# Optimization experiments

Hardware: AMD Instinct MI355X
Metric: run time of the kernel (lower is better)

Reference implementation:

```python
import jax, jax.numpy as jnp
import numpy as np

LN_EPS = 1e-5
NUM_HEADS = 16

def _layernorm(x, g, b):
    mu = jnp.mean(x, axis=-1, keepdims=True)
    var = jnp.mean(jnp.square(x - mu), axis=-1, keepdims=True)
    return (x - mu) * jax.lax.rsqrt(var + LN_EPS) * g + b

def setup_inputs() -> dict:
    key = jax.random.key(0)
    ks = jax.random.split(key, 8)
    B, N, C, Hf = 8, 4096, 1024, 2048
    s = 1.0 / np.sqrt(C)
    return {
        "x": jax.random.normal(ks[0], (B, N, C), jnp.float32),
        "ln1_g": jnp.ones((C,), jnp.float32),
        "ln1_b": jnp.zeros((C,), jnp.float32),
        "ln2_g": jnp.ones((C,), jnp.float32),
        "ln2_b": jnp.zeros((C,), jnp.float32),
        "wq": jax.random.normal(ks[1], (C, C), jnp.float32) * s,
        "wk": jax.random.normal(ks[2], (C, C), jnp.float32) * s,
        "wv": jax.random.normal(ks[3], (C, C), jnp.float32) * s,
        "proj_w": jax.random.normal(ks[4], (C, C), jnp.float32) * s,
        "proj_b": jnp.zeros((C,), jnp.float32),
        "fc1_w": jax.random.normal(ks[5], (C, Hf), jnp.float32) * s,
        "fc1_b": jnp.zeros((Hf,), jnp.float32),
        "fc2_w": jax.random.normal(ks[6], (Hf, C), jnp.float32) / np.sqrt(Hf),
        "fc2_b": jnp.zeros((C,), jnp.float32),
    }

def reference(x, ln1_g, ln1_b, ln2_g, ln2_b, wq, wk, wv, proj_w, proj_b,
              fc1_w, fc1_b, fc2_w, fc2_b):
    B, N, C = x.shape
    H = NUM_HEADS
    d = C // H
    scale = d ** -0.5

    # --- attention branch (note: attention over the head_dim axis, d x d scores) ---
    h = _layernorm(x, ln1_g, ln1_b)
    def split(t):  # (B,N,C) -> (B,H,d,N), matching permute(0,2,3,1)
        return jnp.transpose(t.reshape(B, N, H, d), (0, 2, 3, 1))
    q = split(h @ wq)
    k = split(h @ wk)
    v = split(h @ wv)
    attn = jax.nn.softmax(jnp.einsum("bhdn,bhen->bhde", q, k) * scale, axis=-1)  # (B,H,d,d)
    o = jnp.einsum("bhde,bhen->bhdn", attn, v)           # (B,H,d,N)
    o = jnp.transpose(o, (0, 2, 1, 3)).reshape(B, N, C)  # transpose(1,2).reshape
    x = x + (o @ proj_w + proj_b)

    # --- MLP branch ---
    h2 = _layernorm(x, ln2_g, ln2_b)
    h2 = jax.nn.gelu(h2 @ fc1_w + fc1_b, approximate=False)
    x = x + (h2 @ fc2_w + fc2_b)
    return x
```

## Files before the change

kernel.cpp:

```cpp
#include <hip/hip_runtime.h>
#include <cmath>

typedef __attribute__((ext_vector_type(8))) _Float16 f16x8;
typedef __attribute__((ext_vector_type(8))) unsigned short u16x8;
typedef __attribute__((ext_vector_type(4))) float f32x4;

__device__ __forceinline__ unsigned short f2h(float f) {
  return __builtin_bit_cast(unsigned short, (_Float16)f);
}
__device__ __forceinline__ float h2f(unsigned short u) {
  return (float)__builtin_bit_cast(_Float16, u);
}

__device__ __forceinline__ void async16(const void* gp, void* lp) {
  __builtin_amdgcn_global_load_lds(
      (const __attribute__((address_space(1))) void*)gp,
      (__attribute__((address_space(3))) void*)lp, 16, 0, 0);
}

__global__ __launch_bounds__(256) void transpose_cast(
    const float* __restrict__ W, unsigned short* __restrict__ WT, int K, int N) {
  __shared__ float tile[32][33];
  const int tx = threadIdx.x & 31, ty = threadIdx.x >> 5;
  const int n0 = blockIdx.x * 32, k0 = blockIdx.y * 32;
#pragma unroll
  for (int r = 0; r < 4; ++r)
    tile[ty + 8 * r][tx] = W[(size_t)(k0 + ty + 8 * r) * N + n0 + tx];
  __syncthreads();
#pragma unroll
  for (int r = 0; r < 4; ++r)
    WT[(size_t)(n0 + ty + 8 * r) * K + k0 + tx] = f2h(tile[tx][ty + 8 * r]);
}

__global__ __launch_bounds__(256) void layernorm_cast(
    const float* __restrict__ x, const float* __restrict__ g,
    const float* __restrict__ bt, unsigned short* __restrict__ out) {
  const int row = blockIdx.x, tid = threadIdx.x;
  const float4 v = ((const float4*)(x + (size_t)row * 1024))[tid];
  float s = v.x + v.y + v.z + v.w;
  float ss = v.x * v.x + v.y * v.y + v.z * v.z + v.w * v.w;
#pragma unroll
  for (int off = 32; off >= 1; off >>= 1) {
    s += __shfl_down(s, off);
    ss += __shfl_down(ss, off);
  }
  __shared__ float red[10];
  const int wave = tid >> 6, lane = tid & 63;
  if (lane == 0) { red[wave] = s; red[4 + wave] = ss; }
  __syncthreads();
  if (tid == 0) {
    float S = red[0] + red[1] + red[2] + red[3];
    float SS = red[4] + red[5] + red[6] + red[7];
    float mu = S * (1.f / 1024.f);
    float var = SS * (1.f / 1024.f) - mu * mu;
    red[8] = mu;
    red[9] = rsqrtf(var + 1e-5f);
  }
  __syncthreads();
  const float mu = red[8], rs = red[9];
  const float4 gv = ((const float4*)g)[tid];
  const float4 bv = ((const float4*)bt)[tid];
  ushort4 r;
  r.x = f2h((v.x - mu) * rs * gv.x + bv.x);
  r.y = f2h((v.y - mu) * rs * gv.y + bv.y);
  r.z = f2h((v.z - mu) * rs * gv.z + bv.z);
  r.w = f2h((v.w - mu) * rs * gv.w + bv.w);
  ((ushort4*)(out + (size_t)row * 1024))[tid] = r;
}

__global__ __launch_bounds__(256) void resid_ln(
    const float* __restrict__ x, const unsigned short* __restrict__ pr,
    const float* __restrict__ pb, const float* __restrict__ g,
    const float* __restrict__ bt, float* __restrict__ out,
    unsigned short* __restrict__ h2) {
  const int row = blockIdx.x, tid = threadIdx.x;
  const size_t off = (size_t)row * 1024;
  const float4 xv = ((const float4*)(x + off))[tid];
  const ushort4 pv = ((const ushort4*)(pr + off))[tid];
  const float4 bb = ((const float4*)pb)[tid];
  float4 v;
  v.x = xv.x + h2f(pv.x) + bb.x;
  v.y = xv.y + h2f(pv.y) + bb.y;
  v.z = xv.z + h2f(pv.z) + bb.z;
  v.w = xv.w + h2f(pv.w) + bb.w;
  ((float4*)(out + off))[tid] = v;
  float s = v.x + v.y + v.z + v.w;
  float ss = v.x * v.x + v.y * v.y + v.z * v.z + v.w * v.w;
#pragma unroll
  for (int o = 32; o >= 1; o >>= 1) {
    s += __shfl_down(s, o);
    ss += __shfl_down(ss, o);
  }
  __shared__ float red[10];
  const int wave = tid >> 6, lane = tid & 63;
  if (lane == 0) { red[wave] = s; red[4 + wave] = ss; }
  __syncthreads();
  if (tid == 0) {
    float S = red[0] + red[1] + red[2] + red[3];
    float SS = red[4] + red[5] + red[6] + red[7];
    float mu = S * (1.f / 1024.f);
    float var = SS * (1.f / 1024.f) - mu * mu;
    red[8] = mu;
    red[9] = rsqrtf(var + 1e-5f);
  }
  __syncthreads();
  const float mu = red[8], rs = red[9];
  const float4 gv = ((const float4*)g)[tid];
  const float4 bv = ((const float4*)bt)[tid];
  ushort4 r;
  r.x = f2h((v.x - mu) * rs * gv.x + bv.x);
  r.y = f2h((v.y - mu) * rs * gv.y + bv.y);
  r.z = f2h((v.z - mu) * rs * gv.z + bv.z);
  r.w = f2h((v.w - mu) * rs * gv.w + bv.w);
  ((ushort4*)(h2 + off))[tid] = r;
}

__global__ __launch_bounds__(256) void resid_add(
    float* __restrict__ out, const unsigned short* __restrict__ y,
    const float* __restrict__ b) {
  const int row = blockIdx.x, tid = threadIdx.x;
  const size_t off = (size_t)row * 1024;
  float4 o = ((const float4*)(out + off))[tid];
  const ushort4 yv = ((const ushort4*)(y + off))[tid];
  const float4 bv = ((const float4*)b)[tid];
  o.x += h2f(yv.x) + bv.x;
  o.y += h2f(yv.y) + bv.y;
  o.z += h2f(yv.z) + bv.z;
  o.w += h2f(yv.w) + bv.w;
  ((float4*)(out + off))[tid] = o;
}

__global__ __launch_bounds__(256) void gemm_bt(
    const unsigned short* __restrict__ A, const unsigned short* __restrict__ BT,
    int M, int N, int K,
    const float* __restrict__ bias, unsigned short* __restrict__ outB, int gelu) {
  __shared__ unsigned short smem[17408];
  unsigned short* sA = smem;
  unsigned short* sB = smem + 8192;
  const int tid = threadIdx.x, wave = tid >> 6, lane = tid & 63;
  const int l16 = lane & 15, g16 = lane >> 4;
  const int wm = wave & 1, wn = wave >> 1;

  const int lin = blockIdx.y * gridDim.x + blockIdx.x;
  const int t_ = lin >> 3;
  const int bx = t_ % gridDim.x;
  const int by = (lin & 7) + 8 * (t_ / gridDim.x);
  const int row0 = by * 128, col0 = bx * 128;

  const int r_ = tid >> 2;
  const int s_ = ((tid & 3) ^ ((tid >> 3) & 3)) * 8;
  const unsigned short* pA = A + (size_t)(row0 + r_) * K + s_;
  const unsigned short* pB = BT + (size_t)(col0 + r_) * K + s_;
  unsigned short* dA = sA + wave * 512;
  unsigned short* dB = sB + wave * 512;
  const size_t rstep = (size_t)64 * K;

  f32x4 acc[4][4] = {};

  for (int k0 = 0; k0 < K; k0 += 64) {
    __syncthreads();
    async16(pA, dA);
    async16(pA + rstep, dA + 2048);
    async16(pA + 32, dA + 4096);
    async16(pA + rstep + 32, dA + 6144);
    async16(pB, dB);
    async16(pB + rstep, dB + 2048);
    async16(pB + 32, dB + 4096);
    async16(pB + rstep + 32, dB + 6144);
    pA += 64;
    pB += 64;
    __syncthreads();
#pragma unroll
    for (int kk = 0; kk < 2; ++kk) {
      f16x8 af[4], bf[4];
#pragma unroll
      for (int i = 0; i < 4; ++i) {
        const int ra = wm * 64 + i * 16 + l16;
        af[i] = __builtin_bit_cast(f16x8,
            *(const u16x8*)&sA[kk * 4096 + ra * 32 + (g16 ^ ((ra >> 1) & 3)) * 8]);
      }
#pragma unroll
      for (int j = 0; j < 4; ++j) {
        const int rb = wn * 64 + j * 16 + l16;
        bf[j] = __builtin_bit_cast(f16x8,
            *(const u16x8*)&sB[kk * 4096 + rb * 32 + (g16 ^ ((rb >> 1) & 3)) * 8]);
      }
#pragma unroll
      for (int i = 0; i < 4; ++i)
#pragma unroll
        for (int j = 0; j < 4; ++j)
          acc[i][j] = __builtin_amdgcn_mfma_f32_16x16x32_f16(af[i], bf[j], acc[i][j], 0, 0, 0);
    }
  }

  __syncthreads();
  unsigned short* scr = smem + wave * 4352;
#pragma unroll
  for (int j = 0; j < 4; ++j) {
    const float bcol = gelu ? bias[col0 + wn * 64 + j * 16 + l16] : 0.f;
#pragma unroll
    for (int i = 0; i < 4; ++i)
#pragma unroll
      for (int r = 0; r < 4; ++r) {
        float val = acc[i][j][r] + bcol;
        if (gelu) val = 0.5f * val * (1.0f + erff(val * 0.70710678118f));
        scr[(i * 16 + g16 * 4 + r) * 68 + j * 16 + l16] = f2h(val);
      }
  }
#pragma unroll
  for (int rr = 0; rr < 8; ++rr) {
    const int lr = rr * 8 + (lane >> 3);
    const int lc = (lane & 7) * 8;
    const u16x8 val = *(const u16x8*)&scr[lr * 68 + lc];
    *(u16x8*)(outB + (size_t)(row0 + wm * 64 + lr) * N + col0 + wn * 64 + lc) = val;
  }
}

__global__ __launch_bounds__(256) void attn_qk_part(
    const unsigned short* __restrict__ qkv, float* __restrict__ sp) {
  constexpr int ST = 72;
  __shared__ unsigned short sQT[64 * ST];
  __shared__ unsigned short sKT[64 * ST];
  const int bx = blockIdx.x, bh = bx >> 2, chunk = bx & 3;
  const int b = bh >> 4, h = bh & 15;
  const size_t base = (size_t)b * 4096 * 3072 + (size_t)h * 64;
  const int tid = threadIdx.x, wave = tid >> 6, lane = tid & 63;
  const int l16 = lane & 15, g16 = lane >> 4;
  const int wm = wave & 1, wn = wave >> 1;
  const int srow = tid >> 2, sseg = tid & 3;

  f32x4 acc[2][2] = {};

  for (int ntl = 0; ntl < 16; ++ntl) {
    const int nt = chunk * 16 + ntl;
    __syncthreads();
    const size_t roff = base + (size_t)(nt * 64 + srow) * 3072 + sseg * 16;
    const u16x8 q0 = *(const u16x8*)(qkv + roff);
    const u16x8 q1 = *(const u16x8*)(qkv + roff + 8);
    const u16x8 k0 = *(const u16x8*)(qkv + roff + 1024);
    const u16x8 k1 = *(const u16x8*)(qkv + roff + 1032);
#pragma unroll
    for (int ii = 0; ii < 8; ++ii) {
      sQT[(sseg * 16 + ii) * ST + srow] = q0[ii];
      sQT[(sseg * 16 + 8 + ii) * ST + srow] = q1[ii];
      sKT[(sseg * 16 + ii) * ST + srow] = k0[ii];
      sKT[(sseg * 16 + 8 + ii) * ST + srow] = k1[ii];
    }
    __syncthreads();
#pragma unroll
    for (int kk = 0; kk < 2; ++kk) {
      f16x8 aq[2], bk[2];
#pragma unroll
      for (int i = 0; i < 2; ++i)
        aq[i] = __builtin_bit_cast(f16x8,
            *(const u16x8*)&sQT[(wm * 32 + i * 16 + l16) * ST + kk * 32 + g16 * 8]);
#pragma unroll
      for (int j = 0; j < 2; ++j)
        bk[j] = __builtin_bit_cast(f16x8,
            *(const u16x8*)&sKT[(wn * 32 + j * 16 + l16) * ST + kk * 32 + g16 * 8]);
#pragma unroll
      for (int i = 0; i < 2; ++i)
#pragma unroll
        for (int j = 0; j < 2; ++j)
          acc[i][j] = __builtin_amdgcn_mfma_f32_16x16x32_f16(aq[i], bk[j], acc[i][j], 0, 0, 0);
    }
  }

  float* o = sp + (size_t)bx * 4096;
#pragma unroll
  for (int i = 0; i < 2; ++i)
#pragma unroll
    for (int j = 0; j < 2; ++j)
#pragma unroll
      for (int r = 0; r < 4; ++r)
        o[(wm * 32 + i * 16 + g16 * 4 + r) * 64 + (wn * 32 + j * 16 + l16)] = acc[i][j][r];
}

__global__ __launch_bounds__(64) void attn_softmax(
    const float* __restrict__ sp, unsigned short* __restrict__ am) {
  const int bh = blockIdx.x, dd = threadIdx.x;
  const float* p = sp + (size_t)bh * 4 * 4096 + dd * 64;
  float row[64];
#pragma unroll
  for (int e4 = 0; e4 < 16; ++e4) {
    const float4 a = ((const float4*)p)[e4];
    const float4 b_ = ((const float4*)(p + 4096))[e4];
    const float4 c_ = ((const float4*)(p + 8192))[e4];
    const float4 d_ = ((const float4*)(p + 12288))[e4];
    row[4 * e4 + 0] = a.x + b_.x + c_.x + d_.x;
    row[4 * e4 + 1] = a.y + b_.y + c_.y + d_.y;
    row[4 * e4 + 2] = a.z + b_.z + c_.z + d_.z;
    row[4 * e4 + 3] = a.w + b_.w + c_.w + d_.w;
  }
  float mx = -1e30f;
#pragma unroll
  for (int e = 0; e < 64; ++e) mx = fmaxf(mx, row[e]);
  float sum = 0.f;
#pragma unroll
  for (int e = 0; e < 64; ++e) {
    row[e] = __expf(0.125f * (row[e] - mx));
    sum += row[e];
  }
  const float inv = 1.0f / sum;
  unsigned short* q = am + (size_t)bh * 4096 + dd * 64;
#pragma unroll
  for (int e = 0; e < 64; ++e) q[e] = f2h(row[e] * inv);
}

__global__ __launch_bounds__(256) void attn_pv(
    const unsigned short* __restrict__ qkv, const unsigned short* __restrict__ am,
    unsigned short* __restrict__ o) {
  const int bx = blockIdx.x, bh = bx >> 2, chunk = bx & 3;
  const int b = bh >> 4, h = bh & 15;
  const size_t base = (size_t)b * 4096 * 3072 + (size_t)h * 64;
  const int tid = threadIdx.x, wave = tid >> 6, lane = tid & 63;
  const int l16 = lane & 15, g16 = lane >> 4;
  const int wm = wave & 1, wn = wave >> 1;

  f16x8 amf[2][2];
#pragma unroll
  for (int i = 0; i < 2; ++i)
#pragma unroll
    for (int kk = 0; kk < 2; ++kk)
      amf[i][kk] = __builtin_bit_cast(f16x8,
          *(const u16x8*)(am + (size_t)bh * 4096 +
                          (wm * 32 + i * 16 + l16) * 64 + kk * 32 + g16 * 8));

  for (int ntl = 0; ntl < 16; ++ntl) {
    const int nt = chunk * 16 + ntl;
    f32x4 oc[2][2] = {};
#pragma unroll
    for (int kk = 0; kk < 2; ++kk) {
#pragma unroll
      for (int j = 0; j < 2; ++j) {
        const f16x8 vf = __builtin_bit_cast(f16x8,
            *(const u16x8*)(qkv + base + 2048 +
                            (size_t)(nt * 64 + wn * 32 + j * 16 + l16) * 3072 +
                            kk * 32 + g16 * 8));
#pragma unroll
        for (int i = 0; i < 2; ++i)
          oc[i][j] = __builtin_amdgcn_mfma_f32_16x16x32_f16(amf[i][kk], vf, oc[i][j], 0, 0, 0);
      }
    }
#pragma unroll
    for (int i = 0; i < 2; ++i)
#pragma unroll
      for (int j = 0; j < 2; ++j)
#pragma unroll
        for (int r = 0; r < 4; ++r) {
          const int dd = wm * 32 + i * 16 + g16 * 4 + r;
          const int nf = nt * 64 + wn * 32 + j * 16 + l16;
          const int row = b * 4096 + dd * 64 + h * 4 + (nf >> 10);
          o[(size_t)row * 1024 + (nf & 1023)] = f2h(oc[i][j][r]);
        }
  }
}

extern "C" void kernel_launch(void* const* d_in, const int* in_sizes, int n_in,
                              void* d_out, int out_size, void* d_ws, size_t ws_size,
                              hipStream_t stream) {
  (void)in_sizes; (void)n_in; (void)out_size; (void)ws_size;
  const float* x = (const float*)d_in[0];
  const float* ln1g = (const float*)d_in[1];
  const float* ln1b = (const float*)d_in[2];
  const float* ln2g = (const float*)d_in[3];
  const float* ln2b = (const float*)d_in[4];
  const float* wq = (const float*)d_in[5];
  const float* wk = (const float*)d_in[6];
  const float* wv = (const float*)d_in[7];
  const float* projw = (const float*)d_in[8];
  const float* projb = (const float*)d_in[9];
  const float* fc1w = (const float*)d_in[10];
  const float* fc1b = (const float*)d_in[11];
  const float* fc2w = (const float*)d_in[12];
  const float* fc2b = (const float*)d_in[13];
  float* out = (float*)d_out;

  const int M = 8 * 4096, C = 1024, HF = 2048;
  const size_t MC = (size_t)M * C;

  unsigned short* p = (unsigned short*)d_ws;
  unsigned short* wqkvT = p; p += (size_t)3 * C * C;
  unsigned short* prT = p; p += (size_t)C * C;
  unsigned short* f1T = p; p += (size_t)HF * C;
  unsigned short* f2T = p; p += (size_t)C * HF;
  unsigned short* hb = p;  p += MC;
  unsigned short* qkvb = p; p += 3 * MC;
  float* Spart = (float*)hb;
  unsigned short* Am = wqkvT;
  unsigned short* ob = hb;
  unsigned short* projout = qkvb;
  unsigned short* h2 = qkvb + 2 * MC;
  unsigned short* h3 = qkvb;
  unsigned short* yb = hb;

  transpose_cast<<<dim3(C / 32, C / 32), 256, 0, stream>>>(wq, wqkvT, C, C);
  transpose_cast<<<dim3(C / 32, C / 32), 256, 0, stream>>>(wk, wqkvT + (size_t)C * C, C, C);
  transpose_cast<<<dim3(C / 32, C / 32), 256, 0, stream>>>(wv, wqkvT + (size_t)2 * C * C, C, C);
  transpose_cast<<<dim3(C / 32, C / 32), 256, 0, stream>>>(projw, prT, C, C);
  transpose_cast<<<dim3(HF / 32, C / 32), 256, 0, stream>>>(fc1w, f1T, C, HF);
  transpose_cast<<<dim3(C / 32, HF / 32), 256, 0, stream>>>(fc2w, f2T, HF, C);

  layernorm_cast<<<M, 256, 0, stream>>>(x, ln1g, ln1b, hb);

  gemm_bt<<<dim3(3 * C / 128, M / 128), 256, 0, stream>>>(
      hb, wqkvT, M, 3 * C, C, nullptr, qkvb, 0);

  attn_qk_part<<<512, 256, 0, stream>>>(qkvb, Spart);
  attn_softmax<<<128, 64, 0, stream>>>(Spart, Am);
  attn_pv<<<512, 256, 0, stream>>>(qkvb, Am, ob);

  gemm_bt<<<dim3(C / 128, M / 128), 256, 0, stream>>>(
      ob, prT, M, C, C, nullptr, projout, 0);

  resid_ln<<<M, 256, 0, stream>>>(x, projout, projb, ln2g, ln2b, out, h2);

  gemm_bt<<<dim3(HF / 128, M / 128), 256, 0, stream>>>(
      h2, f1T, M, HF, C, fc1b, h3, 1);

  gemm_bt<<<dim3(C / 128, M / 128), 256, 0, stream>>>(
      h3, f2T, M, C, HF, nullptr, yb, 0);

  resid_add<<<M, 256, 0, stream>>>(out, yb, fc2b);
}
```

Baseline: 1.173 ms.

## Add 256x256-tile pipelined GEMM kernel for MLP fc1/fc2

Adds a new 512-thread GEMM kernel with 256x256 output tiles. It uses a double-buffered LDS pipeline fed by async global-to-LDS loads, swizzled LDS layout, block-index remapping for L2 locality, and setprio around the MFMA bursts. The two MLP GEMMs now launch this kernel instead of the 128x128 one, aiming for more data reuse per tile and better overlap of loads with compute. The larger tile uses 128KB of LDS and many accumulator registers, which limits occupancy, and it yields fewer blocks for the N=1024 fc2 GEMM.

```diff
diff --git a/kernel.cpp b/kernel.cpp
--- a/kernel.cpp
+++ b/kernel.cpp
@@ -213,6 +213,146 @@
     const int lc = (lane & 7) * 8;
     const u16x8 val = *(const u16x8*)&scr[lr * 68 + lc];
     *(u16x8*)(outB + (size_t)(row0 + wm * 64 + lr) * N + col0 + wn * 64 + lc) = val;
+  }
+}
+
+
+#define STAGE_A(TT, KKH)                                                       \
+  {                                                                            \
+    unsigned short* d = smem + ((TT) & 1) * 32768 + (KKH) * 8192 + wave * 512; \
+    const unsigned short* sp_ = pA + (size_t)(TT) * 64 + (KKH) * 32;           \
+    async16(sp_, d);                                                           \
+    async16(sp_ + rstep, d + 4096);                                            \
+  }
+
+#define STAGE_B(TT, KKH)                                                       \
+  {                                                                            \
+    unsigned short* d =                                                        \
+        smem + ((TT) & 1) * 32768 + 16384 + (KKH) * 8192 + wave * 512;         \
+    const unsigned short* sp_ = pB + (size_t)(TT) * 64 + (KKH) * 32;           \
+    async16(sp_, d);                                                           \
+    async16(sp_ + rstep, d + 4096);                                            \
+  }
+
+#define GPHASE(KK, MH, STAGE, TAILW)                                           \
+  {                                                                            \
+    f16x8 af[4];                                                               \
+    _Pragma("unroll") for (int i = 0; i < 4; ++i) {                            \
+      const int ra = wm * 128 + ((MH)*4 + i) * 16 + l16;                       \
+      af[i] = __builtin_bit_cast(                                              \
+          f16x8, *(const u16x8*)&bufA[(KK)*8192 + ra * 32 +                    \
+                                      ((g16 ^ ((ra >> 1) & 3)) * 8)]);         \
+    }                                                                          \
+    if ((MH) == 0) {                                                           \
+      _Pragma("unroll") for (int j = 0; j < 4; ++j) {                          \
+        const int rb = wn * 64 + j * 16 + l16;                                 \
+        bf[j] = __builtin_bit_cast(                                            \
+            f16x8, *(const u16x8*)&bufB[(KK)*8192 + rb * 32 +                  \
+                                        ((g16 ^ ((rb >> 1) & 3)) * 8)]);       \
+      }                                                                        \
+    }                                                                          \
+    STAGE;                                                                     \
+    __builtin_amdgcn_s_barrier();                                              \
+    asm volatile("s_waitcnt lgkmcnt(0)" ::: "memory");                         \
+    __builtin_amdgcn_s_setprio(1);                                             \
+    _Pragma("unroll") for (int i = 0; i < 4; ++i)                              \
+        _Pragma("unroll") for (int j = 0; j < 4; ++j) acc[(MH)*4 + i][j] =     \
+        __builtin_amdgcn_mfma_f32_16x16x32_f16(af[i], bf[j],                   \
+                                               acc[(MH)*4 + i][j], 0, 0, 0);   \
+    __builtin_amdgcn_s_setprio(0);                                             \
+    TAILW;                                                                     \
+    __builtin_amdgcn_s_barrier();                                              \
+  }
+
+__global__ __launch_bounds__(512) void gemm256(
+    const unsigned short* __restrict__ A, const unsigned short* __restrict__ BT,
+    int M, int N, int K,
+    const float* __restrict__ bias, unsigned short* __restrict__ outB, int gelu) {
+  __shared__ __align__(16) unsigned short smem[65536];
+  const int tid = threadIdx.x, wave = tid >> 6, lane = tid & 63;
+  const int l16 = lane & 15, g16 = lane >> 4;
+  const int wm = wave >> 2, wn = wave & 3;
+
+  const int lin = blockIdx.y * gridDim.x + blockIdx.x;
+  const int t_ = lin >> 3;
+  const int bx = t_ % gridDim.x;
+  const int by = (lin & 7) + 8 * (t_ / gridDim.x);
+  const int row0 = by * 256, col0 = bx * 256;
+
+  const int r_ = tid >> 2;
+  const int s_ = ((tid & 3) ^ ((tid >> 3) & 3)) * 8;
+  const unsigned short* pA = A + (size_t)(row0 + r_) * K + s_;
+  const unsigned short* pB = BT + (size_t)(col0 + r_) * K + s_;
+  const size_t rstep = (size_t)128 * K;
+  const int NT = K >> 6;
+
+  f32x4 acc[8][4] = {};
+
+  STAGE_B(0, 0);
+  STAGE_A(0, 0);
+  STAGE_B(0, 1);
+  STAGE_A(0, 1);
+  STAGE_B(1, 0);
+  STAGE_A(1, 0);
+  STAGE_B(1, 1);
+  asm volatile("s_waitcnt vmcnt(6)" ::: "memory");
+  __builtin_amdgcn_s_barrier();
+
+  for (int t = 0; t < NT - 2; ++t) {
+    const unsigned short* bufA = smem + (t & 1) * 32768;
+    const unsigned short* bufB = bufA + 16384;
+    f16x8 bf[4];
+    GPHASE(0, 0, STAGE_A(t + 1, 1), )
+    GPHASE(0, 1, STAGE_B(t + 2, 0), )
+    GPHASE(1, 0, STAGE_A(t + 2, 0), )
+    GPHASE(1, 1, STAGE_B(t + 2, 1),
+           asm volatile("s_waitcnt vmcnt(6)" ::: "memory"))
+  }
+
+  {
+    const int t = NT - 2;
+    const unsigned short* bufA = smem + (t & 1) * 32768;
+    const unsigned short* bufB = bufA + 16384;
+    f16x8 bf[4];
+    GPHASE(0, 0, STAGE_A(t + 1, 1), )
+    GPHASE(0, 1, , )
+    GPHASE(1, 0, , )
+    GPHASE(1, 1, , asm volatile("s_waitcnt vmcnt(0)" ::: "memory"))
+  }
+  {
+    const int t = NT - 1;
+    const unsigned short* bufA = smem + (t & 1) * 32768;
+    const unsigned short* bufB = bufA + 16384;
+    f16x8 bf[4];
+    GPHASE(0, 0, , )
+    GPHASE(0, 1, , )
+    GPHASE(1, 0, , )
+    GPHASE(1, 1, , )
+  }
+
+  unsigned short* scr = smem + wave * 4352;
+#pragma unroll
+  for (int mh = 0; mh < 2; ++mh) {
+#pragma unroll
+    for (int j = 0; j < 4; ++j) {
+      const float bcol = gelu ? bias[col0 + wn * 64 + j * 16 + l16] : 0.f;
+#pragma unroll
+      for (int i = 0; i < 4; ++i)
+#pragma unroll
+        for (int r = 0; r < 4; ++r) {
+          float val = acc[mh * 4 + i][j][r] + bcol;
+          if (gelu) val = 0.5f * val * (1.0f + erff(val * 0.70710678118f));
+          scr[(i * 16 + g16 * 4 + r) * 68 + j * 16 + l16] = f2h(val);
+        }
+    }
+#pragma unroll
+    for (int rr = 0; rr < 8; ++rr) {
+      const int lr = rr * 8 + (lane >> 3);
+      const int lc = (lane & 7) * 8;
+      const u16x8 val = *(const u16x8*)&scr[lr * 68 + lc];
+      *(u16x8*)(outB + (size_t)(row0 + wm * 128 + mh * 64 + lr) * N + col0 +
+                wn * 64 + lc) = val;
+    }
   }
 }
 
@@ -415,10 +555,10 @@
 
   resid_ln<<<M, 256, 0, stream>>>(x, projout, projb, ln2g, ln2b, out, h2);
 
-  gemm_bt<<<dim3(HF / 128, M / 128), 256, 0, stream>>>(
+  gemm256<<<dim3(HF / 256, M / 256), 512, 0, stream>>>(
       h2, f1T, M, HF, C, fc1b, h3, 1);
 
-  gemm_bt<<<dim3(C / 128, M / 128), 256, 0, stream>>>(
+  gemm256<<<dim3(C / 256, M / 256), 512, 0, stream>>>(
       h3, f2T, M, C, HF, nullptr, yb, 0);
 
   resid_add<<<M, 256, 0, stream>>>(out, yb, fc2b);
```

After: 1.173 ms. No clear change (+0.0%).
